# Kernel tuning notes

Hardware: AMD Instinct MI355X
Metric: run time of the kernel (lower is better)

## Reference

```python
import jax, jax.numpy as jnp
import numpy as np

B, SS, T, D, H = 512, 4, 64, 300, 256  # batch, sentences/sample, words/sentence, wordvec, hidden


def setup_inputs() -> dict:
    key = jax.random.key(0)
    ks = jax.random.split(key, 17)
    s = 0.05
    rn = lambda k, shape: (jax.random.normal(k, shape, jnp.float32) * s)
    return dict(
        x=jax.random.normal(ks[0], (B, SS, T, D), jnp.float32),
        # gru1: GRU(300 -> 256), PyTorch gate order (r, z, n)
        w_ih1=rn(ks[1], (3 * H, D)), w_hh1=rn(ks[2], (3 * H, H)),
        b_ih1=rn(ks[3], (3 * H,)), b_hh1=rn(ks[4], (3 * H,)),
        # gru2: bidirectional GRU(256 -> 256), forward + backward directions
        w_ih2f=rn(ks[5], (3 * H, H)), w_hh2f=rn(ks[6], (3 * H, H)),
        b_ih2f=rn(ks[7], (3 * H,)), b_hh2f=rn(ks[8], (3 * H,)),
        w_ih2b=rn(ks[9], (3 * H, H)), w_hh2b=rn(ks[10], (3 * H, H)),
        b_ih2b=rn(ks[11], (3 * H,)), b_hh2b=rn(ks[12], (3 * H,)),
        # classifier: Linear(512,256) -> LeakyReLU(0.1) -> Linear(256,2)
        wc1=rn(ks[13], (H, 2 * H)), bc1=rn(ks[14], (H,)),
        wc2=rn(ks[15], (2, H)), bc2=rn(ks[16], (2,)),
    )


def _gru_final_hidden(x, w_ih, w_hh, b_ih, b_hh):
    # x: [N, T, D] -> final hidden state [N, H]; PyTorch GRU math, gate order r,z,n
    xg = jnp.einsum('ntd,gd->tng', x, w_ih) + b_ih  # [T, N, 3H], input gates precomputed
    h0 = jnp.zeros((x.shape[0], w_hh.shape[1]), x.dtype)

    def step(h, xg_t):
        hg = h @ w_hh.T + b_hh
        xr, xz, xn = jnp.split(xg_t, 3, axis=-1)
        hr, hz, hn = jnp.split(hg, 3, axis=-1)
        r = jax.nn.sigmoid(xr + hr)
        z = jax.nn.sigmoid(xz + hz)
        n = jnp.tanh(xn + r * hn)
        return (1.0 - z) * n + z * h, None

    hT, _ = jax.lax.scan(step, h0, xg)
    return hT


def _gru_cell_zero_h(x, w_ih, b_ih, b_hh):
    # gru2 is called with seq_len=1 and h0=0, so each direction is one cell step
    # (W_hh @ 0 == 0, only the hidden biases survive)
    xg = x @ w_ih.T + b_ih
    xr, xz, xn = jnp.split(xg, 3, axis=-1)
    br, bz, bn = jnp.split(b_hh, 3)
    r = jax.nn.sigmoid(xr + br)
    z = jax.nn.sigmoid(xz + bz)
    n = jnp.tanh(xn + r * bn)
    return (1.0 - z) * n


def reference(x, w_ih1, w_hh1, b_ih1, b_hh1,
              w_ih2f, w_hh2f, b_ih2f, b_hh2f,
              w_ih2b, w_hh2b, b_ih2b, b_hh2b,
              wc1, bc1, wc2, bc2):
    Bn, S, Tn, Dn = x.shape
    # integrate_words: gru1 over each sentence's words, keep final hidden
    h1 = _gru_final_hidden(x.reshape(Bn * S, Tn, Dn), w_ih1, w_hh1, b_ih1, b_hh1)
    h1 = h1.reshape(Bn, S, -1)  # [B, SS, H]
    # integrate_sentences: bidir gru2 with batch=SS, seq_len=1; out[SS//2] is kept,
    # and with seq_len=1 that output depends only on the middle sentence's embedding
    mid = h1[:, S // 2, :]  # [B, H]
    hf = _gru_cell_zero_h(mid, w_ih2f, b_ih2f, b_hh2f)
    hb = _gru_cell_zero_h(mid, w_ih2b, b_ih2b, b_hh2b)
    emb = jnp.concatenate([hf, hb], axis=-1)  # [B, 2H]
    pre = emb @ wc1.T + bc1
    hidden = jnp.where(pre >= 0, pre, 0.1 * pre)  # LeakyReLU(0.1)
    logits = hidden @ wc2.T + bc2  # [B, 2]
    return logits
```

## Files before the change

kernel.cpp:

```cpp
#include <hip/hip_runtime.h>
#include <hip/hip_bf16.h>

typedef unsigned short u16;
typedef unsigned int u32;
using short8 = __attribute__((ext_vector_type(8))) short;
using f32x4  = __attribute__((ext_vector_type(4))) float;

#define T_   64
#define D_   300
#define H_   256
#define G_   768
#define NROW 512
#define M_   (NROW * T_)
#define KP_  320

__device__ __forceinline__ float bf2f(u16 v) {
    union { u32 u; float f; } x; x.u = ((u32)v) << 16; return x.f;
}
__device__ __forceinline__ float bf2f_lo(u32 w) {
    union { u32 u; float f; } x; x.u = w << 16; return x.f;
}
__device__ __forceinline__ float bf2f_hi(u32 w) {
    union { u32 u; float f; } x; x.u = w & 0xFFFF0000u; return x.f;
}
__device__ __forceinline__ u16 f2bf(float f) {
    union { u32 u; float f; } x; x.f = f;
    u32 u = x.u;
    u32 r = (u + 0x7FFFu + ((u >> 16) & 1u)) >> 16;
    return (u16)r;
}
__device__ __forceinline__ float frcp(float x) {
    float r; asm("v_rcp_f32 %0, %1" : "=v"(r) : "v"(x)); return r;
}
__device__ __forceinline__ float fsigm(float x) { return frcp(1.f + __expf(-x)); }
__device__ __forceinline__ float ftanh(float x) {
    return 1.f - 2.f * frcp(1.f + __expf(2.f * x));
}
__device__ __forceinline__ float sigm(float x) { return 1.f / (1.f + expf(-x)); }

__global__ __launch_bounds__(256) void kx_cast(
    const float* __restrict__ x, u16* __restrict__ xb)
{
    const int gid = blockIdx.x * 256 + threadIdx.x;
    const int row = gid / 40, seg = gid - row * 40;
    const int k0 = seg * 8;
    const int n = row >> 6, t = row & 63;
    const float* src = x + (size_t)(n * 256 + 128 + t) * D_;
    union { u16 h[8]; uint4 q; } u;
    if (k0 + 8 <= D_) {
        const float4 a = *reinterpret_cast<const float4*>(src + k0);
        const float4 b = *reinterpret_cast<const float4*>(src + k0 + 4);
        u.h[0] = f2bf(a.x); u.h[1] = f2bf(a.y); u.h[2] = f2bf(a.z); u.h[3] = f2bf(a.w);
        u.h[4] = f2bf(b.x); u.h[5] = f2bf(b.y); u.h[6] = f2bf(b.z); u.h[7] = f2bf(b.w);
    } else {
#pragma unroll
        for (int e = 0; e < 8; ++e)
            u.h[e] = (k0 + e < D_) ? f2bf(src[k0 + e]) : (u16)0;
    }
    *reinterpret_cast<uint4*>(&xb[(size_t)row * KP_ + k0]) = u.q;
}

__global__ __launch_bounds__(256) void k0_prep(
    const float* __restrict__ w_ih1, const float* __restrict__ w_hh1,
    const float* __restrict__ b_ih1, const float* __restrict__ b_hh1,
    const float* __restrict__ w2f, const float* __restrict__ w2b,
    const float* __restrict__ wc1,
    u16* __restrict__ wihb, u16* __restrict__ whpk,
    u16* __restrict__ w2ft, u16* __restrict__ w2bt, u16* __restrict__ wc1t,
    float* __restrict__ biasc)
{
    int y = blockIdx.y;
    int tid = blockIdx.x * 256 + threadIdx.x;
    if (y == 0) {
        if (tid < G_ * KP_) {
            int g = tid / KP_, k = tid % KP_;
            wihb[tid] = (k < D_) ? f2bf(w_ih1[g * D_ + k]) : (u16)0;
        }
    } else if (y == 1) {
        if (tid < 48 * 8 * 64) {
            int lane = tid & 63;
            int ks = (tid >> 6) & 7;
            int nt = tid >> 9;
            int g  = nt * 16 + (lane & 15);
            int kb = ks * 32 + ((lane >> 4) << 3);
            union { u16 h[8]; uint4 q; } u;
#pragma unroll
            for (int e = 0; e < 8; ++e) u.h[e] = f2bf(w_hh1[g * H_ + kb + e]);
            *reinterpret_cast<uint4*>(&whpk[(size_t)tid * 8]) = u.q;
        }
    } else if (y == 2 || y == 3) {
        if (tid < G_ * H_) {
            int k = tid / G_, g = tid % G_;
            const float* src = (y == 2) ? w2f : w2b;
            u16* dst = (y == 2) ? w2ft : w2bt;
            dst[tid] = f2bf(src[g * H_ + k]);
        }
    } else {
        if (tid < 512 * 256) {
            int k = tid / 256, o = tid % 256;
            wc1t[tid] = f2bf(wc1[o * 512 + k]);
        }
        if (tid < G_)
            biasc[tid] = b_ih1[tid] + (tid < 2 * H_ ? b_hh1[tid] : 0.f);
    }
}

__global__ __launch_bounds__(256) void k1_xgemm(
    const u16* __restrict__ xb, const u16* __restrict__ wihb,
    const float* __restrict__ biasc, u32* __restrict__ xgw)
{
    __shared__ alignas(16) u16 As[128 * 40];
    __shared__ alignas(16) u16 Bs[128 * 40];
    const int tid = threadIdx.x;
    const int l = tid & 63, wv = tid >> 6;
    const int wrow = wv >> 1, wcol = wv & 1;
    const int row0 = blockIdx.x * 128, col0 = blockIdx.y * 128;

    f32x4 acc[4][4];
#pragma unroll
    for (int i = 0; i < 4; ++i)
#pragma unroll
        for (int j = 0; j < 4; ++j) acc[i][j] = (f32x4){0.f, 0.f, 0.f, 0.f};

    const int ar = tid >> 1, ah = tid & 1;
    const u16* xrow  = xb + (size_t)(row0 + ar) * KP_;
    const u16* wrowp = wihb + (size_t)(col0 + ar) * KP_;

    for (int k0 = 0; k0 < KP_; k0 += 32) {
        *reinterpret_cast<uint4*>(&As[ar * 40 + ah * 16]) =
            *reinterpret_cast<const uint4*>(xrow + k0 + ah * 16);
        *reinterpret_cast<uint4*>(&As[ar * 40 + ah * 16 + 8]) =
            *reinterpret_cast<const uint4*>(xrow + k0 + ah * 16 + 8);
        *reinterpret_cast<uint4*>(&Bs[ar * 40 + ah * 16]) =
            *reinterpret_cast<const uint4*>(wrowp + k0 + ah * 16);
        *reinterpret_cast<uint4*>(&Bs[ar * 40 + ah * 16 + 8]) =
            *reinterpret_cast<const uint4*>(wrowp + k0 + ah * 16 + 8);
        __syncthreads();

        short8 af[4], bf[4];
#pragma unroll
        for (int fi = 0; fi < 4; ++fi)
            af[fi] = *reinterpret_cast<const short8*>(
                &As[(wrow * 64 + fi * 16 + (l & 15)) * 40 + ((l >> 4) << 3)]);
#pragma unroll
        for (int fj = 0; fj < 4; ++fj)
            bf[fj] = *reinterpret_cast<const short8*>(
                &Bs[(wcol * 64 + fj * 16 + (l & 15)) * 40 + ((l >> 4) << 3)]);
#pragma unroll
        for (int fi = 0; fi < 4; ++fi)
#pragma unroll
            for (int fj = 0; fj < 4; ++fj)
                acc[fi][fj] = __builtin_amdgcn_mfma_f32_16x16x32_bf16(
                    af[fi], bf[fj], acc[fi][fj], 0, 0, 0);
        __syncthreads();
    }

    float bias[4];
#pragma unroll
    for (int fj = 0; fj < 4; ++fj)
        bias[fj] = biasc[col0 + wcol * 64 + fj * 16 + (l & 15)];
#pragma unroll
    for (int fi = 0; fi < 4; ++fi)
#pragma unroll
        for (int fjp = 0; fjp < 2; ++fjp) {
            const int cg0 = col0 + wcol * 64 + fjp * 32;
            const int g = cg0 >> 8;
            const int wv8 = (cg0 & 255) >> 5;
            const int word = g * 128 + wv8 * 16 + (l & 15);
#pragma unroll
            for (int q = 0; q < 4; ++q) {
                const int row = row0 + wrow * 64 + fi * 16 + ((l >> 4) << 2) + q;
                const int t = row & 63, n = row >> 6;
                const u32 lo = f2bf(acc[fi][2 * fjp][q] + bias[2 * fjp]);
                const u32 hi = f2bf(acc[fi][2 * fjp + 1][q] + bias[2 * fjp + 1]);
                xgw[((size_t)t * NROW + n) * 384 + word] = lo | (hi << 16);
            }
        }
}

__global__ __launch_bounds__(512)
__attribute__((amdgpu_waves_per_eu(2, 2)))
void k2_gru(const u32* __restrict__ xgw, const u16* __restrict__ whpk,
            const float* __restrict__ b_hh, float* __restrict__ mid)
{
    extern __shared__ u16 smem[];
    u16* wl = smem;
    u16* hb = smem + 48 * 2 * 64 * 8;
    const int tid = threadIdx.x;
    const int l = tid & 63, wv = tid >> 6;
    const int n0 = blockIdx.x * 8;
    const int c = l & 15, rgrp = l >> 4;
    const int arow = c, klo = rgrp << 3;
    const int aSel = rgrp >> 1;
    const int rbase = (rgrp & 1) * 4;
    const int u = wv * 32 + aSel * 16 + c;

    short8 wr[6][6];
#pragma unroll
    for (int gt = 0; gt < 3; ++gt)
#pragma unroll
        for (int a = 0; a < 2; ++a) {
            const int nt = gt * 16 + wv * 2 + a;
#pragma unroll
            for (int ks = 0; ks < 6; ++ks)
                wr[gt * 2 + a][ks] = *reinterpret_cast<const short8*>(
                    &whpk[(size_t)((nt * 8 + ks) * 64 + l) * 8]);
        }
    asm volatile("" :
        "+a"(wr[0][0]),"+a"(wr[0][1]),"+a"(wr[0][2]),"+a"(wr[0][3]),"+a"(wr[0][4]),"+a"(wr[0][5]),
        "+a"(wr[1][0]),"+a"(wr[1][1]),"+a"(wr[1][2]),"+a"(wr[1][3]),"+a"(wr[1][4]),"+a"(wr[1][5]),
        "+a"(wr[2][0]),"+a"(wr[2][1]),"+a"(wr[2][2]),"+a"(wr[2][3]),"+a"(wr[2][4]),"+a"(wr[2][5]));
    asm volatile("" :
        "+a"(wr[3][0]),"+a"(wr[3][1]),"+a"(wr[3][2]),"+a"(wr[3][3]),"+a"(wr[3][4]),"+a"(wr[3][5]),
        "+a"(wr[4][0]),"+a"(wr[4][1]),"+a"(wr[4][2]),"+a"(wr[4][3]),"+a"(wr[4][4]),"+a"(wr[4][5]),
        "+a"(wr[5][0]),"+a"(wr[5][1]),"+a"(wr[5][2]),"+a"(wr[5][3]),"+a"(wr[5][4]),"+a"(wr[5][5]));

    for (int cc = tid; cc < 48 * 2 * 64; cc += 512) {
        const int nt = cc >> 7, j = (cc >> 6) & 1, ll = cc & 63;
        *reinterpret_cast<uint4*>(&wl[(size_t)cc * 8]) =
            *reinterpret_cast<const uint4*>(
                &whpk[(size_t)((nt * 8 + 6 + j) * 64 + ll) * 8]);
    }
    for (int i = tid; i < 2 * 16 * 264 / 2; i += 512) ((u32*)hb)[i] = 0;

    const float bhn = b_hh[512 + u];
    u32 xo[4];
#pragma unroll
    for (int q = 0; q < 4; ++q)
        xo[q] = (u32)(n0 + rbase + q) * 384 + wv * 16 + c;
    float h[4] = {0.f, 0.f, 0.f, 0.f};
    const u32 stepw = (u32)NROW * 384;

    u32 xa[3][4], xn2[3][4];
#pragma unroll
    for (int q = 0; q < 4; ++q) {
        xa[0][q] = xgw[xo[q]];
        xa[1][q] = xgw[xo[q] + 128];
        xa[2][q] = xgw[xo[q] + 256];
    }

    __syncthreads();

    int p = 0;
    for (int t = 0; t < T_; ++t) {
        const u32 tb = (u32)(t + 1 < T_ ? t + 1 : T_ - 1) * stepw;
#pragma unroll
        for (int q = 0; q < 4; ++q) {
            xn2[0][q] = xgw[tb + xo[q]];
            xn2[1][q] = xgw[tb + xo[q] + 128];
            xn2[2][q] = xgw[tb + xo[q] + 256];
        }

        const u16* hbr = hb + p * (16 * 264);
        f32x4 acc[6];
#pragma unroll
        for (int m = 0; m < 6; ++m) acc[m] = (f32x4){0.f, 0.f, 0.f, 0.f};
        __builtin_amdgcn_s_setprio(1);
#pragma unroll
        for (int ks = 0; ks < 6; ++ks) {
            const short8 afr = *reinterpret_cast<const short8*>(
                &hbr[arow * 264 + ks * 32 + klo]);
#pragma unroll
            for (int m = 0; m < 6; ++m)
                acc[m] = __builtin_amdgcn_mfma_f32_16x16x32_bf16(
                    afr, wr[m][ks], acc[m], 0, 0, 0);
        }
#pragma unroll
        for (int ks = 6; ks < 8; ++ks) {
            const short8 afr = *reinterpret_cast<const short8*>(
                &hbr[arow * 264 + ks * 32 + klo]);
#pragma unroll
            for (int gt = 0; gt < 3; ++gt)
#pragma unroll
                for (int a = 0; a < 2; ++a) {
                    const int nt2 = (gt * 16 + wv * 2 + a) * 2 + (ks - 6);
                    const short8 bfr = *reinterpret_cast<const short8*>(
                        &wl[(size_t)(nt2 * 64 + l) * 8]);
                    acc[gt * 2 + a] = __builtin_amdgcn_mfma_f32_16x16x32_bf16(
                        afr, bfr, acc[gt * 2 + a], 0, 0, 0);
                }
        }
        __builtin_amdgcn_s_setprio(0);

        float vr[4], vz[4], vn[4];
#pragma unroll
        for (int q = 0; q < 4; ++q) {
            const float r1 = __shfl(acc[1][q], l & 31);
            const float z1 = __shfl(acc[3][q], l & 31);
            const float n1 = __shfl(acc[5][q], l & 31);
            vr[q] = (l < 32) ? acc[0][q] : r1;
            vz[q] = (l < 32) ? acc[2][q] : z1;
            vn[q] = (l < 32) ? acc[4][q] : n1;
        }

        u16* hbw = hb + (p ^ 1) * (16 * 264);
#pragma unroll
        for (int q = 0; q < 4; ++q) {
            const float xr = aSel ? bf2f_hi(xa[0][q]) : bf2f_lo(xa[0][q]);
            const float xz = aSel ? bf2f_hi(xa[1][q]) : bf2f_lo(xa[1][q]);
            const float xn = aSel ? bf2f_hi(xa[2][q]) : bf2f_lo(xa[2][q]);
            const float rg = fsigm(xr + vr[q]);
            const float zg = fsigm(xz + vz[q]);
            const float ng = ftanh(xn + rg * (vn[q] + bhn));
            h[q] = zg * (h[q] - ng) + ng;
            hbw[(rbase + q) * 264 + u] = f2bf(h[q]);
        }

#pragma unroll
        for (int g = 0; g < 3; ++g)
#pragma unroll
            for (int q = 0; q < 4; ++q) xa[g][q] = xn2[g][q];

        asm volatile("s_waitcnt lgkmcnt(0)" ::: "memory");
        __builtin_amdgcn_sched_barrier(0);
        __builtin_amdgcn_s_barrier();
        __builtin_amdgcn_sched_barrier(0);
        p ^= 1;
    }

#pragma unroll
    for (int q = 0; q < 4; ++q)
        mid[(size_t)(n0 + rbase + q) * H_ + u] = h[q];
}

__global__ __launch_bounds__(256) void k3_head(
    const float* __restrict__ mid,
    const u16* __restrict__ w2ft, const u16* __restrict__ w2bt,
    const float* __restrict__ b_ih2f, const float* __restrict__ b_hh2f,
    const float* __restrict__ b_ih2b, const float* __restrict__ b_hh2b,
    const u16* __restrict__ wc1t, const float* __restrict__ bc1,
    const float* __restrict__ wc2, const float* __restrict__ bc2,
    float* __restrict__ out)
{
    __shared__ float m[4][H_];
    __shared__ float xg2[2][4][G_];
    __shared__ float emb[4][512];
    __shared__ float hid[4][H_];
    int tid = threadIdx.x;
    int r0 = blockIdx.x * 4;

    for (int i = tid; i < 4 * H_; i += 256) {
        int r = i >> 8, k = i & 255;
        m[r][k] = mid[(size_t)(r0 + r) * H_ + k];
    }
    __syncthreads();

    const int g0 = tid, g1 = tid + 256, g2 = tid + 512;
    float bf0 = b_ih2f[g0] + b_hh2f[g0];
    float bf1 = b_ih2f[g1] + b_hh2f[g1];
    float bf2v = b_ih2f[g2];
    float bb0 = b_ih2b[g0] + b_hh2b[g0];
    float bb1 = b_ih2b[g1] + b_hh2b[g1];
    float bb2v = b_ih2b[g2];
    float af[4][3], ab[4][3];
#pragma unroll
    for (int r = 0; r < 4; ++r) {
        af[r][0] = bf0; af[r][1] = bf1; af[r][2] = bf2v;
        ab[r][0] = bb0; ab[r][1] = bb1; ab[r][2] = bb2v;
    }
#pragma unroll 4
    for (int k = 0; k < H_; ++k) {
        float wf0 = bf2f(w2ft[k * G_ + g0]);
        float wf1 = bf2f(w2ft[k * G_ + g1]);
        float wf2 = bf2f(w2ft[k * G_ + g2]);
        float wb0 = bf2f(w2bt[k * G_ + g0]);
        float wb1 = bf2f(w2bt[k * G_ + g1]);
        float wb2 = bf2f(w2bt[k * G_ + g2]);
#pragma unroll
        for (int r = 0; r < 4; ++r) {
            float mm = m[r][k];
            af[r][0] += mm * wf0; af[r][1] += mm * wf1; af[r][2] += mm * wf2;
            ab[r][0] += mm * wb0; ab[r][1] += mm * wb1; ab[r][2] += mm * wb2;
        }
    }
#pragma unroll
    for (int r = 0; r < 4; ++r) {
        xg2[0][r][g0] = af[r][0]; xg2[0][r][g1] = af[r][1]; xg2[0][r][g2] = af[r][2];
        xg2[1][r][g0] = ab[r][0]; xg2[1][r][g1] = ab[r][1]; xg2[1][r][g2] = ab[r][2];
    }
    __syncthreads();

    {
        const int j = tid;
        float bnf = b_hh2f[512 + j], bnb = b_hh2b[512 + j];
#pragma unroll
        for (int r = 0; r < 4; ++r) {
            float rg = sigm(xg2[0][r][j]);
            float zg = sigm(xg2[0][r][256 + j]);
            float ng = tanhf(xg2[0][r][512 + j] + rg * bnf);
            emb[r][j] = (1.f - zg) * ng;
            rg = sigm(xg2[1][r][j]);
            zg = sigm(xg2[1][r][256 + j]);
            ng = tanhf(xg2[1][r][512 + j] + rg * bnb);
            emb[r][256 + j] = (1.f - zg) * ng;
        }
    }
    __syncthreads();

    {
        const int o = tid;
        float acc[4];
        float b = bc1[o];
#pragma unroll
        for (int r = 0; r < 4; ++r) acc[r] = b;
#pragma unroll 4
        for (int k = 0; k < 512; ++k) {
            float w = bf2f(wc1t[k * H_ + o]);
#pragma unroll
            for (int r = 0; r < 4; ++r) acc[r] += emb[r][k] * w;
        }
#pragma unroll
        for (int r = 0; r < 4; ++r) {
            float pre = acc[r];
            hid[r][o] = pre >= 0.f ? pre : 0.1f * pre;
        }
    }
    __syncthreads();

    {
        int grp = tid >> 5, lane = tid & 31;
        int r = grp >> 1, cc = grp & 1;
        float s = 0.f;
        for (int k = lane; k < H_; k += 32) s += hid[r][k] * wc2[cc * H_ + k];
#pragma unroll
        for (int msk = 16; msk >= 1; msk >>= 1) s += __shfl_xor(s, msk, 32);
        if (lane == 0) out[(size_t)(r0 + r) * 2 + cc] = s + bc2[cc];
    }
}

extern "C" void kernel_launch(void* const* d_in, const int* in_sizes, int n_in,
                              void* d_out, int out_size, void* d_ws, size_t ws_size,
                              hipStream_t stream)
{
    const float* x      = (const float*)d_in[0];
    const float* w_ih1  = (const float*)d_in[1];
    const float* w_hh1  = (const float*)d_in[2];
    const float* b_ih1  = (const float*)d_in[3];
    const float* b_hh1  = (const float*)d_in[4];
    const float* w_ih2f = (const float*)d_in[5];
    const float* b_ih2f = (const float*)d_in[7];
    const float* b_hh2f = (const float*)d_in[8];
    const float* w_ih2b = (const float*)d_in[9];
    const float* b_ih2b = (const float*)d_in[11];
    const float* b_hh2b = (const float*)d_in[12];
    const float* wc1    = (const float*)d_in[13];
    const float* bc1    = (const float*)d_in[14];
    const float* wc2    = (const float*)d_in[15];
    const float* bc2    = (const float*)d_in[16];
    float* out = (float*)d_out;

    char* p = (char*)d_ws;
    u32* xgw  = (u32*)p;  p += (size_t)M_ * 384 * 4;
    u16* xb   = (u16*)p;  p += (size_t)M_ * KP_ * 2;
    u16* wihb = (u16*)p;  p += (size_t)G_ * KP_ * 2;
    u16* whpk = (u16*)p;  p += (size_t)48 * 8 * 64 * 8 * 2;
    u16* w2ft = (u16*)p;  p += (size_t)G_ * H_ * 2;
    u16* w2bt = (u16*)p;  p += (size_t)G_ * H_ * 2;
    u16* wc1t = (u16*)p;  p += (size_t)512 * 256 * 2;
    float* mid = (float*)p; p += (size_t)NROW * H_ * 4;
    float* biasc = (float*)p; p += (size_t)G_ * 4;

    kx_cast<<<M_ * 40 / 256, 256, 0, stream>>>(x, xb);
    k0_prep<<<dim3(960, 5), 256, 0, stream>>>(w_ih1, w_hh1, b_ih1, b_hh1,
                                              w_ih2f, w_ih2b, wc1,
                                              wihb, whpk, w2ft, w2bt, wc1t, biasc);
    k1_xgemm<<<dim3(M_ / 128, G_ / 128), 256, 0, stream>>>(xb, wihb, biasc, xgw);
    const int k2_lds = (48 * 2 * 64 * 8 + 2 * 16 * 264) * 2;
    k2_gru<<<64, 512, k2_lds, stream>>>(xgw, whpk, b_hh1, mid);
    k3_head<<<128, 256, 0, stream>>>(mid, w2ft, w2bt, b_ih2f, b_hh2f,
                                     b_ih2b, b_hh2b, wc1t, bc1, wc2, bc2, out);
}
```

Baseline: 233.7 us.

## Double-buffer input GEMM with K=64 stages and drop GRU gate shuffles

The input-projection GEMM now uses two LDS buffers with 64-wide K stages. Global loads for the next stage are prefetched into registers while MFMAs run on the current one, which cuts barrier count and overlaps memory with compute. In the recurrent kernel, the cross-lane shuffles that gathered upper-half accumulators are removed: lanes 0-31 compute both hidden units directly from acc[0..5] while lanes 32-63 sit idle in the elementwise phase. That doubles the serial gate math per active lane but removes the shuffle and select instructions from every time step.

```diff
diff --git a/kernel.cpp b/kernel.cpp
--- a/kernel.cpp
+++ b/kernel.cpp
@@ -105,16 +105,17 @@
     }
 }
 
-__global__ __launch_bounds__(256) void k1_xgemm(
+__global__ __launch_bounds__(256, 2) void k1_xgemm(
     const u16* __restrict__ xb, const u16* __restrict__ wihb,
     const float* __restrict__ biasc, u32* __restrict__ xgw)
 {
-    __shared__ alignas(16) u16 As[128 * 40];
-    __shared__ alignas(16) u16 Bs[128 * 40];
+    __shared__ alignas(16) u16 As[2][128][72];
+    __shared__ alignas(16) u16 Bs[2][128][72];
     const int tid = threadIdx.x;
     const int l = tid & 63, wv = tid >> 6;
     const int wrow = wv >> 1, wcol = wv & 1;
     const int row0 = blockIdx.x * 128, col0 = blockIdx.y * 128;
+    const int ar = tid >> 1, ah = tid & 1;
 
     f32x4 acc[4][4];
 #pragma unroll
@@ -122,36 +123,52 @@
 #pragma unroll
         for (int j = 0; j < 4; ++j) acc[i][j] = (f32x4){0.f, 0.f, 0.f, 0.f};
 
-    const int ar = tid >> 1, ah = tid & 1;
-    const u16* xrow  = xb + (size_t)(row0 + ar) * KP_;
-    const u16* wrowp = wihb + (size_t)(col0 + ar) * KP_;
-
-    for (int k0 = 0; k0 < KP_; k0 += 32) {
-        *reinterpret_cast<uint4*>(&As[ar * 40 + ah * 16]) =
-            *reinterpret_cast<const uint4*>(xrow + k0 + ah * 16);
-        *reinterpret_cast<uint4*>(&As[ar * 40 + ah * 16 + 8]) =
-            *reinterpret_cast<const uint4*>(xrow + k0 + ah * 16 + 8);
-        *reinterpret_cast<uint4*>(&Bs[ar * 40 + ah * 16]) =
-            *reinterpret_cast<const uint4*>(wrowp + k0 + ah * 16);
-        *reinterpret_cast<uint4*>(&Bs[ar * 40 + ah * 16 + 8]) =
-            *reinterpret_cast<const uint4*>(wrowp + k0 + ah * 16 + 8);
-        __syncthreads();
-
-        short8 af[4], bf[4];
-#pragma unroll
-        for (int fi = 0; fi < 4; ++fi)
-            af[fi] = *reinterpret_cast<const short8*>(
-                &As[(wrow * 64 + fi * 16 + (l & 15)) * 40 + ((l >> 4) << 3)]);
-#pragma unroll
-        for (int fj = 0; fj < 4; ++fj)
-            bf[fj] = *reinterpret_cast<const short8*>(
-                &Bs[(wcol * 64 + fj * 16 + (l & 15)) * 40 + ((l >> 4) << 3)]);
-#pragma unroll
-        for (int fi = 0; fi < 4; ++fi)
+    const u16* xrow  = xb + (size_t)(row0 + ar) * KP_ + ah * 32;
+    const u16* wrowp = wihb + (size_t)(col0 + ar) * KP_ + ah * 32;
+
+    uint4 ra[4], rb[4];
+    auto loadregs = [&](int it) {
+        const int k0 = it * 64;
+#pragma unroll
+        for (int e = 0; e < 4; ++e) {
+            ra[e] = *reinterpret_cast<const uint4*>(xrow + k0 + e * 8);
+            rb[e] = *reinterpret_cast<const uint4*>(wrowp + k0 + e * 8);
+        }
+    };
+    auto writelds = [&](int buf) {
+#pragma unroll
+        for (int e = 0; e < 4; ++e) {
+            *reinterpret_cast<uint4*>(&As[buf][ar][ah * 32 + e * 8]) = ra[e];
+            *reinterpret_cast<uint4*>(&Bs[buf][ar][ah * 32 + e * 8]) = rb[e];
+        }
+    };
+
+    loadregs(0);
+    writelds(0);
+    __syncthreads();
+
+    for (int it = 0; it < 5; ++it) {
+        const int cur = it & 1;
+        if (it < 4) loadregs(it + 1);
+#pragma unroll
+        for (int kc = 0; kc < 2; ++kc) {
+            short8 af[4], bf[4];
+#pragma unroll
+            for (int fi = 0; fi < 4; ++fi)
+                af[fi] = *reinterpret_cast<const short8*>(
+                    &As[cur][wrow * 64 + fi * 16 + (l & 15)][kc * 32 + ((l >> 4) << 3)]);
 #pragma unroll
             for (int fj = 0; fj < 4; ++fj)
-                acc[fi][fj] = __builtin_amdgcn_mfma_f32_16x16x32_bf16(
-                    af[fi], bf[fj], acc[fi][fj], 0, 0, 0);
+                bf[fj] = *reinterpret_cast<const short8*>(
+                    &Bs[cur][wcol * 64 + fj * 16 + (l & 15)][kc * 32 + ((l >> 4) << 3)]);
+#pragma unroll
+            for (int fi = 0; fi < 4; ++fi)
+#pragma unroll
+                for (int fj = 0; fj < 4; ++fj)
+                    acc[fi][fj] = __builtin_amdgcn_mfma_f32_16x16x32_bf16(
+                        af[fi], bf[fj], acc[fi][fj], 0, 0, 0);
+        }
+        if (it < 4) writelds(cur ^ 1);
         __syncthreads();
     }
 
@@ -191,9 +208,8 @@
     const int n0 = blockIdx.x * 8;
     const int c = l & 15, rgrp = l >> 4;
     const int arow = c, klo = rgrp << 3;
-    const int aSel = rgrp >> 1;
     const int rbase = (rgrp & 1) * 4;
-    const int u = wv * 32 + aSel * 16 + c;
+    const int u0 = wv * 32 + c;
 
     short8 wr[6][6];
 #pragma unroll
@@ -223,32 +239,38 @@
     }
     for (int i = tid; i < 2 * 16 * 264 / 2; i += 512) ((u32*)hb)[i] = 0;
 
-    const float bhn = b_hh[512 + u];
+    const float bhn0 = b_hh[512 + u0];
+    const float bhn1 = b_hh[512 + u0 + 16];
     u32 xo[4];
 #pragma unroll
     for (int q = 0; q < 4; ++q)
         xo[q] = (u32)(n0 + rbase + q) * 384 + wv * 16 + c;
-    float h[4] = {0.f, 0.f, 0.f, 0.f};
+    float h0[4] = {0.f, 0.f, 0.f, 0.f};
+    float h1[4] = {0.f, 0.f, 0.f, 0.f};
     const u32 stepw = (u32)NROW * 384;
 
     u32 xa[3][4], xn2[3][4];
-#pragma unroll
-    for (int q = 0; q < 4; ++q) {
-        xa[0][q] = xgw[xo[q]];
-        xa[1][q] = xgw[xo[q] + 128];
-        xa[2][q] = xgw[xo[q] + 256];
+    if (l < 32) {
+#pragma unroll
+        for (int q = 0; q < 4; ++q) {
+            xa[0][q] = xgw[xo[q]];
+            xa[1][q] = xgw[xo[q] + 128];
+            xa[2][q] = xgw[xo[q] + 256];
+        }
     }
 
     __syncthreads();
 
     int p = 0;
     for (int t = 0; t < T_; ++t) {
-        const u32 tb = (u32)(t + 1 < T_ ? t + 1 : T_ - 1) * stepw;
-#pragma unroll
-        for (int q = 0; q < 4; ++q) {
-            xn2[0][q] = xgw[tb + xo[q]];
-            xn2[1][q] = xgw[tb + xo[q] + 128];
-            xn2[2][q] = xgw[tb + xo[q] + 256];
+        if (l < 32) {
+            const u32 tb = (u32)(t + 1 < T_ ? t + 1 : T_ - 1) * stepw;
+#pragma unroll
+            for (int q = 0; q < 4; ++q) {
+                xn2[0][q] = xgw[tb + xo[q]];
+                xn2[1][q] = xgw[tb + xo[q] + 128];
+                xn2[2][q] = xgw[tb + xo[q] + 256];
+            }
         }
 
         const u16* hbr = hb + p * (16 * 264);
@@ -282,34 +304,27 @@
         }
         __builtin_amdgcn_s_setprio(0);
 
-        float vr[4], vz[4], vn[4];
-#pragma unroll
-        for (int q = 0; q < 4; ++q) {
-            const float r1 = __shfl(acc[1][q], l & 31);
-            const float z1 = __shfl(acc[3][q], l & 31);
-            const float n1 = __shfl(acc[5][q], l & 31);
-            vr[q] = (l < 32) ? acc[0][q] : r1;
-            vz[q] = (l < 32) ? acc[2][q] : z1;
-            vn[q] = (l < 32) ? acc[4][q] : n1;
-        }
-
         u16* hbw = hb + (p ^ 1) * (16 * 264);
-#pragma unroll
-        for (int q = 0; q < 4; ++q) {
-            const float xr = aSel ? bf2f_hi(xa[0][q]) : bf2f_lo(xa[0][q]);
-            const float xz = aSel ? bf2f_hi(xa[1][q]) : bf2f_lo(xa[1][q]);
-            const float xn = aSel ? bf2f_hi(xa[2][q]) : bf2f_lo(xa[2][q]);
-            const float rg = fsigm(xr + vr[q]);
-            const float zg = fsigm(xz + vz[q]);
-            const float ng = ftanh(xn + rg * (vn[q] + bhn));
-            h[q] = zg * (h[q] - ng) + ng;
-            hbw[(rbase + q) * 264 + u] = f2bf(h[q]);
-        }
-
-#pragma unroll
-        for (int g = 0; g < 3; ++g)
-#pragma unroll
-            for (int q = 0; q < 4; ++q) xa[g][q] = xn2[g][q];
+        if (l < 32) {
+#pragma unroll
+            for (int q = 0; q < 4; ++q) {
+                const float rg0 = fsigm(bf2f_lo(xa[0][q]) + acc[0][q]);
+                const float zg0 = fsigm(bf2f_lo(xa[1][q]) + acc[2][q]);
+                const float ng0 = ftanh(bf2f_lo(xa[2][q]) + rg0 * (acc[4][q] + bhn0));
+                h0[q] = zg0 * (h0[q] - ng0) + ng0;
+                hbw[(rbase + q) * 264 + u0] = f2bf(h0[q]);
+
+                const float rg1 = fsigm(bf2f_hi(xa[0][q]) + acc[1][q]);
+                const float zg1 = fsigm(bf2f_hi(xa[1][q]) + acc[3][q]);
+                const float ng1 = ftanh(bf2f_hi(xa[2][q]) + rg1 * (acc[5][q] + bhn1));
+                h1[q] = zg1 * (h1[q] - ng1) + ng1;
+                hbw[(rbase + q) * 264 + u0 + 16] = f2bf(h1[q]);
+            }
+#pragma unroll
+            for (int g = 0; g < 3; ++g)
+#pragma unroll
+                for (int q = 0; q < 4; ++q) xa[g][q] = xn2[g][q];
+        }
 
         asm volatile("s_waitcnt lgkmcnt(0)" ::: "memory");
         __builtin_amdgcn_sched_barrier(0);
@@ -318,9 +333,13 @@
         p ^= 1;
     }
 
-#pragma unroll
-    for (int q = 0; q < 4; ++q)
-        mid[(size_t)(n0 + rbase + q) * H_ + u] = h[q];
+    if (l < 32) {
+#pragma unroll
+        for (int q = 0; q < 4; ++q) {
+            mid[(size_t)(n0 + rbase + q) * H_ + u0] = h0[q];
+            mid[(size_t)(n0 + rbase + q) * H_ + u0 + 16] = h1[q];
+        }
+    }
 }
 
 __global__ __launch_bounds__(256) void k3_head(
```

After: 299.0 us. 27.9% more time.

## Hold all recurrent GRU weights in registers with 4 waves per 16 rows

Applied to the files above, without the earlier changes.

The recurrent GRU kernel moves from 64 blocks of 512 threads (8 rows each, with part of W_hh staged in LDS) to 32 blocks of 256 threads covering 16 rows each. Every wave now keeps its full K=256 slice of W_hh in registers: the r/z gate tiles in AGPRs and the n gate tiles in VGPRs. This removes the per-step LDS weight reads and the cross-lane shuffles used to combine half-tile results. In exchange each wave issues twice as many MFMAs per step, the launch uses half as many CUs, and the code runs at one wave per EU under heavy register pressure. The prefetch of the next step's input gates is also moved after the gate math.

```diff
diff --git a/kernel.cpp b/kernel.cpp
--- a/kernel.cpp
+++ b/kernel.cpp
@@ -16,12 +16,6 @@
 
 __device__ __forceinline__ float bf2f(u16 v) {
     union { u32 u; float f; } x; x.u = ((u32)v) << 16; return x.f;
-}
-__device__ __forceinline__ float bf2f_lo(u32 w) {
-    union { u32 u; float f; } x; x.u = w << 16; return x.f;
-}
-__device__ __forceinline__ float bf2f_hi(u32 w) {
-    union { u32 u; float f; } x; x.u = w & 0xFFFF0000u; return x.f;
 }
 __device__ __forceinline__ u16 f2bf(float f) {
     union { u32 u; float f; } x; x.f = f;
@@ -178,138 +172,139 @@
         }
 }
 
-__global__ __launch_bounds__(512)
-__attribute__((amdgpu_waves_per_eu(2, 2)))
+__global__ __launch_bounds__(256)
+__attribute__((amdgpu_waves_per_eu(1, 1)))
 void k2_gru(const u32* __restrict__ xgw, const u16* __restrict__ whpk,
             const float* __restrict__ b_hh, float* __restrict__ mid)
 {
-    extern __shared__ u16 smem[];
-    u16* wl = smem;
-    u16* hb = smem + 48 * 2 * 64 * 8;
+    __shared__ u16 hb[2][16 * 264];
     const int tid = threadIdx.x;
     const int l = tid & 63, wv = tid >> 6;
-    const int n0 = blockIdx.x * 8;
+    const int n0 = blockIdx.x * 16;
     const int c = l & 15, rgrp = l >> 4;
     const int arow = c, klo = rgrp << 3;
-    const int aSel = rgrp >> 1;
-    const int rbase = (rgrp & 1) * 4;
-    const int u = wv * 32 + aSel * 16 + c;
-
-    short8 wr[6][6];
-#pragma unroll
-    for (int gt = 0; gt < 3; ++gt)
-#pragma unroll
-        for (int a = 0; a < 2; ++a) {
-            const int nt = gt * 16 + wv * 2 + a;
-#pragma unroll
-            for (int ks = 0; ks < 6; ++ks)
-                wr[gt * 2 + a][ks] = *reinterpret_cast<const short8*>(
-                    &whpk[(size_t)((nt * 8 + ks) * 64 + l) * 8]);
-        }
-    asm volatile("" :
-        "+a"(wr[0][0]),"+a"(wr[0][1]),"+a"(wr[0][2]),"+a"(wr[0][3]),"+a"(wr[0][4]),"+a"(wr[0][5]),
-        "+a"(wr[1][0]),"+a"(wr[1][1]),"+a"(wr[1][2]),"+a"(wr[1][3]),"+a"(wr[1][4]),"+a"(wr[1][5]),
-        "+a"(wr[2][0]),"+a"(wr[2][1]),"+a"(wr[2][2]),"+a"(wr[2][3]),"+a"(wr[2][4]),"+a"(wr[2][5]));
-    asm volatile("" :
-        "+a"(wr[3][0]),"+a"(wr[3][1]),"+a"(wr[3][2]),"+a"(wr[3][3]),"+a"(wr[3][4]),"+a"(wr[3][5]),
-        "+a"(wr[4][0]),"+a"(wr[4][1]),"+a"(wr[4][2]),"+a"(wr[4][3]),"+a"(wr[4][4]),"+a"(wr[4][5]),
-        "+a"(wr[5][0]),"+a"(wr[5][1]),"+a"(wr[5][2]),"+a"(wr[5][3]),"+a"(wr[5][4]),"+a"(wr[5][5]));
-
-    for (int cc = tid; cc < 48 * 2 * 64; cc += 512) {
-        const int nt = cc >> 7, j = (cc >> 6) & 1, ll = cc & 63;
-        *reinterpret_cast<uint4*>(&wl[(size_t)cc * 8]) =
-            *reinterpret_cast<const uint4*>(
-                &whpk[(size_t)((nt * 8 + 6 + j) * 64 + ll) * 8]);
-    }
-    for (int i = tid; i < 2 * 16 * 264 / 2; i += 512) ((u32*)hb)[i] = 0;
-
-    const float bhn = b_hh[512 + u];
+
+    short8 wa[8][8];
+#pragma unroll
+    for (int m = 0; m < 8; ++m) {
+        const int nt = (m >> 2) * 16 + 4 * wv + (m & 3);
+#pragma unroll
+        for (int ks = 0; ks < 8; ++ks)
+            wa[m][ks] = *reinterpret_cast<const short8*>(
+                &whpk[(size_t)((nt * 8 + ks) * 64 + l) * 8]);
+    }
+    short8 wn[4][8];
+#pragma unroll
+    for (int m = 0; m < 4; ++m) {
+        const int nt = 32 + 4 * wv + m;
+#pragma unroll
+        for (int ks = 0; ks < 8; ++ks)
+            wn[m][ks] = *reinterpret_cast<const short8*>(
+                &whpk[(size_t)((nt * 8 + ks) * 64 + l) * 8]);
+    }
+    asm volatile("" :
+        "+a"(wa[0][0]),"+a"(wa[0][1]),"+a"(wa[0][2]),"+a"(wa[0][3]),
+        "+a"(wa[0][4]),"+a"(wa[0][5]),"+a"(wa[0][6]),"+a"(wa[0][7]),
+        "+a"(wa[1][0]),"+a"(wa[1][1]),"+a"(wa[1][2]),"+a"(wa[1][3]),
+        "+a"(wa[1][4]),"+a"(wa[1][5]),"+a"(wa[1][6]),"+a"(wa[1][7]));
+    asm volatile("" :
+        "+a"(wa[2][0]),"+a"(wa[2][1]),"+a"(wa[2][2]),"+a"(wa[2][3]),
+        "+a"(wa[2][4]),"+a"(wa[2][5]),"+a"(wa[2][6]),"+a"(wa[2][7]),
+        "+a"(wa[3][0]),"+a"(wa[3][1]),"+a"(wa[3][2]),"+a"(wa[3][3]),
+        "+a"(wa[3][4]),"+a"(wa[3][5]),"+a"(wa[3][6]),"+a"(wa[3][7]));
+    asm volatile("" :
+        "+a"(wa[4][0]),"+a"(wa[4][1]),"+a"(wa[4][2]),"+a"(wa[4][3]),
+        "+a"(wa[4][4]),"+a"(wa[4][5]),"+a"(wa[4][6]),"+a"(wa[4][7]),
+        "+a"(wa[5][0]),"+a"(wa[5][1]),"+a"(wa[5][2]),"+a"(wa[5][3]),
+        "+a"(wa[5][4]),"+a"(wa[5][5]),"+a"(wa[5][6]),"+a"(wa[5][7]));
+    asm volatile("" :
+        "+a"(wa[6][0]),"+a"(wa[6][1]),"+a"(wa[6][2]),"+a"(wa[6][3]),
+        "+a"(wa[6][4]),"+a"(wa[6][5]),"+a"(wa[6][6]),"+a"(wa[6][7]),
+        "+a"(wa[7][0]),"+a"(wa[7][1]),"+a"(wa[7][2]),"+a"(wa[7][3]),
+        "+a"(wa[7][4]),"+a"(wa[7][5]),"+a"(wa[7][6]),"+a"(wa[7][7]));
+    asm volatile("" :
+        "+v"(wn[0][0]),"+v"(wn[0][1]),"+v"(wn[0][2]),"+v"(wn[0][3]),
+        "+v"(wn[0][4]),"+v"(wn[0][5]),"+v"(wn[0][6]),"+v"(wn[0][7]),
+        "+v"(wn[1][0]),"+v"(wn[1][1]),"+v"(wn[1][2]),"+v"(wn[1][3]),
+        "+v"(wn[1][4]),"+v"(wn[1][5]),"+v"(wn[1][6]),"+v"(wn[1][7]));
+    asm volatile("" :
+        "+v"(wn[2][0]),"+v"(wn[2][1]),"+v"(wn[2][2]),"+v"(wn[2][3]),
+        "+v"(wn[2][4]),"+v"(wn[2][5]),"+v"(wn[2][6]),"+v"(wn[2][7]),
+        "+v"(wn[3][0]),"+v"(wn[3][1]),"+v"(wn[3][2]),"+v"(wn[3][3]),
+        "+v"(wn[3][4]),"+v"(wn[3][5]),"+v"(wn[3][6]),"+v"(wn[3][7]));
+
+    for (int i = tid; i < 2 * 16 * 264 / 2; i += 256)
+        reinterpret_cast<u32*>(hb)[i] = 0;
+
+    float bhn[4];
+#pragma unroll
+    for (int j = 0; j < 4; ++j)
+        bhn[j] = b_hh[512 + 64 * wv + 16 * j + c];
     u32 xo[4];
 #pragma unroll
     for (int q = 0; q < 4; ++q)
-        xo[q] = (u32)(n0 + rbase + q) * 384 + wv * 16 + c;
-    float h[4] = {0.f, 0.f, 0.f, 0.f};
+        xo[q] = (u32)(n0 + rgrp * 4 + q) * 384 + c;
+    float h[4][4] = {};
     const u32 stepw = (u32)NROW * 384;
 
-    u32 xa[3][4], xn2[3][4];
-#pragma unroll
-    for (int q = 0; q < 4; ++q) {
-        xa[0][q] = xgw[xo[q]];
-        xa[1][q] = xgw[xo[q] + 128];
-        xa[2][q] = xgw[xo[q] + 256];
-    }
+    u32 xw[3][2][4];
+#pragma unroll
+    for (int q = 0; q < 4; ++q)
+#pragma unroll
+        for (int g = 0; g < 3; ++g)
+#pragma unroll
+            for (int pp = 0; pp < 2; ++pp)
+                xw[g][pp][q] = xgw[xo[q] + g * 128 + (2 * wv + pp) * 16];
 
     __syncthreads();
 
     int p = 0;
     for (int t = 0; t < T_; ++t) {
-        const u32 tb = (u32)(t + 1 < T_ ? t + 1 : T_ - 1) * stepw;
-#pragma unroll
-        for (int q = 0; q < 4; ++q) {
-            xn2[0][q] = xgw[tb + xo[q]];
-            xn2[1][q] = xgw[tb + xo[q] + 128];
-            xn2[2][q] = xgw[tb + xo[q] + 256];
-        }
-
-        const u16* hbr = hb + p * (16 * 264);
-        f32x4 acc[6];
-#pragma unroll
-        for (int m = 0; m < 6; ++m) acc[m] = (f32x4){0.f, 0.f, 0.f, 0.f};
+        const u16* hbr = hb[p];
+        f32x4 acc[12];
+#pragma unroll
+        for (int m = 0; m < 12; ++m) acc[m] = (f32x4){0.f, 0.f, 0.f, 0.f};
         __builtin_amdgcn_s_setprio(1);
 #pragma unroll
-        for (int ks = 0; ks < 6; ++ks) {
+        for (int ks = 0; ks < 8; ++ks) {
             const short8 afr = *reinterpret_cast<const short8*>(
                 &hbr[arow * 264 + ks * 32 + klo]);
 #pragma unroll
-            for (int m = 0; m < 6; ++m)
+            for (int m = 0; m < 8; ++m)
                 acc[m] = __builtin_amdgcn_mfma_f32_16x16x32_bf16(
-                    afr, wr[m][ks], acc[m], 0, 0, 0);
-        }
-#pragma unroll
-        for (int ks = 6; ks < 8; ++ks) {
-            const short8 afr = *reinterpret_cast<const short8*>(
-                &hbr[arow * 264 + ks * 32 + klo]);
-#pragma unroll
-            for (int gt = 0; gt < 3; ++gt)
-#pragma unroll
-                for (int a = 0; a < 2; ++a) {
-                    const int nt2 = (gt * 16 + wv * 2 + a) * 2 + (ks - 6);
-                    const short8 bfr = *reinterpret_cast<const short8*>(
-                        &wl[(size_t)(nt2 * 64 + l) * 8]);
-                    acc[gt * 2 + a] = __builtin_amdgcn_mfma_f32_16x16x32_bf16(
-                        afr, bfr, acc[gt * 2 + a], 0, 0, 0);
-                }
+                    afr, wa[m][ks], acc[m], 0, 0, 0);
+#pragma unroll
+            for (int m = 0; m < 4; ++m)
+                acc[8 + m] = __builtin_amdgcn_mfma_f32_16x16x32_bf16(
+                    afr, wn[m][ks], acc[8 + m], 0, 0, 0);
         }
         __builtin_amdgcn_s_setprio(0);
 
-        float vr[4], vz[4], vn[4];
-#pragma unroll
-        for (int q = 0; q < 4; ++q) {
-            const float r1 = __shfl(acc[1][q], l & 31);
-            const float z1 = __shfl(acc[3][q], l & 31);
-            const float n1 = __shfl(acc[5][q], l & 31);
-            vr[q] = (l < 32) ? acc[0][q] : r1;
-            vz[q] = (l < 32) ? acc[2][q] : z1;
-            vn[q] = (l < 32) ? acc[4][q] : n1;
-        }
-
-        u16* hbw = hb + (p ^ 1) * (16 * 264);
-#pragma unroll
-        for (int q = 0; q < 4; ++q) {
-            const float xr = aSel ? bf2f_hi(xa[0][q]) : bf2f_lo(xa[0][q]);
-            const float xz = aSel ? bf2f_hi(xa[1][q]) : bf2f_lo(xa[1][q]);
-            const float xn = aSel ? bf2f_hi(xa[2][q]) : bf2f_lo(xa[2][q]);
-            const float rg = fsigm(xr + vr[q]);
-            const float zg = fsigm(xz + vz[q]);
-            const float ng = ftanh(xn + rg * (vn[q] + bhn));
-            h[q] = zg * (h[q] - ng) + ng;
-            hbw[(rbase + q) * 264 + u] = f2bf(h[q]);
-        }
-
-#pragma unroll
-        for (int g = 0; g < 3; ++g)
-#pragma unroll
-            for (int q = 0; q < 4; ++q) xa[g][q] = xn2[g][q];
+        u16* hbw = hb[p ^ 1];
+#pragma unroll
+        for (int j = 0; j < 4; ++j) {
+            const int pw = j >> 1, shv = (j & 1) << 4;
+#pragma unroll
+            for (int q = 0; q < 4; ++q) {
+                const float xr = bf2f((u16)(xw[0][pw][q] >> shv));
+                const float xz = bf2f((u16)(xw[1][pw][q] >> shv));
+                const float xn = bf2f((u16)(xw[2][pw][q] >> shv));
+                const float rg = fsigm(xr + acc[j][q]);
+                const float zg = fsigm(xz + acc[4 + j][q]);
+                const float ng = ftanh(xn + rg * (acc[8 + j][q] + bhn[j]));
+                h[j][q] = zg * (h[j][q] - ng) + ng;
+                hbw[(rgrp * 4 + q) * 264 + 64 * wv + 16 * j + c] = f2bf(h[j][q]);
+            }
+        }
+
+        const u32 tb = (u32)(t + 1 < T_ ? t + 1 : T_ - 1) * stepw;
+#pragma unroll
+        for (int q = 0; q < 4; ++q)
+#pragma unroll
+            for (int g = 0; g < 3; ++g)
+#pragma unroll
+                for (int pp = 0; pp < 2; ++pp)
+                    xw[g][pp][q] = xgw[tb + xo[q] + g * 128 + (2 * wv + pp) * 16];
 
         asm volatile("s_waitcnt lgkmcnt(0)" ::: "memory");
         __builtin_amdgcn_sched_barrier(0);
@@ -319,8 +314,10 @@
     }
 
 #pragma unroll
-    for (int q = 0; q < 4; ++q)
-        mid[(size_t)(n0 + rbase + q) * H_ + u] = h[q];
+    for (int j = 0; j < 4; ++j)
+#pragma unroll
+        for (int q = 0; q < 4; ++q)
+            mid[(size_t)(n0 + rgrp * 4 + q) * H_ + 64 * wv + 16 * j + c] = h[j][q];
 }
 
 __global__ __launch_bounds__(256) void k3_head(
@@ -465,8 +462,7 @@
                                               w_ih2f, w_ih2b, wc1,
                                               wihb, whpk, w2ft, w2bt, wc1t, biasc);
     k1_xgemm<<<dim3(M_ / 128, G_ / 128), 256, 0, stream>>>(xb, wihb, biasc, xgw);
-    const int k2_lds = (48 * 2 * 64 * 8 + 2 * 16 * 264) * 2;
-    k2_gru<<<64, 512, k2_lds, stream>>>(xgw, whpk, b_hh1, mid);
+    k2_gru<<<32, 256, 0, stream>>>(xgw, whpk, b_hh1, mid);
     k3_head<<<128, 256, 0, stream>>>(mid, w2ft, w2bt, b_ih2f, b_hh2f,
                                      b_ih2b, b_hh2b, wc1t, bc1, wc2, bc2, out);
 }
```

Result: slower. 268.6 us (+14.9%).
